# Kernel optimization log

Hardware: AMD Instinct MI355X
Metric: run time of the kernel (lower is better)

Reference implementation:

```python
import jax, jax.numpy as jnp
import numpy as np

NUM_EMBEDDINGS = 1024
EMBEDDING_DIM = 64
COMMITMENT_COST = 0.25


def setup_inputs() -> dict:
    key = jax.random.key(0)
    k1, k2 = jax.random.split(key)
    inputs = jax.random.normal(k1, (16, EMBEDDING_DIM, 64, 64), dtype=jnp.float32)  # NCHW
    embedding = jax.random.normal(k2, (NUM_EMBEDDINGS, EMBEDDING_DIM), dtype=jnp.float32)
    return {"inputs": inputs, "embedding": embedding}


def reference(inputs, embedding):
    # NCHW -> NHWC, flatten to [N, d]
    x = jnp.transpose(inputs, (0, 2, 3, 1))  # [B,H,W,d]
    in_shape = x.shape
    flat = x.reshape(-1, EMBEDDING_DIM)  # [N, d]

    distances = (
        jnp.sum(flat * flat, axis=1, keepdims=True)
        + jnp.sum(embedding * embedding, axis=1)
        - 2.0 * flat @ embedding.T
    )  # [N, K]
    encoding_indices = jnp.argmin(distances, axis=1)  # [N]

    # one-hot @ embedding == gather (avoid materializing [N, K] one-hot)
    quantized = embedding[encoding_indices].reshape(in_shape)  # [B,H,W,d]

    # commitment loss (quantized detached)
    e_latent_loss = jnp.mean((jax.lax.stop_gradient(quantized) - x) ** 2)
    loss = COMMITMENT_COST * e_latent_loss

    # straight-through estimator
    quantized_st = x + jax.lax.stop_gradient(quantized - x)
    quantized_out = jnp.transpose(quantized_st, (0, 3, 1, 2))  # back to NCHW

    return loss, quantized_out, encoding_indices[:, None]
```

## Files before the change

kernel.cpp:

```cpp
#include <hip/hip_runtime.h>


#define DIMS   64
#define HW     4096
#define NPTS   65536
#define NCODES 1024
#define NPB    128
#define QOFF   1
#define IOFF   (1 + NPTS * DIMS)
#define EPSGAP 1.0e-3f

typedef unsigned int uint;
typedef unsigned short ushort;
typedef unsigned long long ull;
typedef __attribute__((ext_vector_type(8))) short short8;
typedef __attribute__((ext_vector_type(16))) float f32x16;

__device__ __forceinline__ ushort bf16_rne(float f) {
    uint u = __float_as_uint(f);
    uint r = u + 0x7FFFu + ((u >> 16) & 1u);
    return (ushort)(r >> 16);
}
__device__ __forceinline__ float bf16f(ushort h) { return __uint_as_float(((uint)h) << 16); }

__device__ __forceinline__ void gload16(const void* g, void* l) {
    __builtin_amdgcn_global_load_lds(
        (const __attribute__((address_space(1))) void*)g,
        (__attribute__((address_space(3))) void*)l, 16, 0, 0);
}

__global__ void vq_prep(const float* __restrict__ emb, ushort* __restrict__ Eh,
                        ushort* __restrict__ El, float* __restrict__ hsq,
                        float* __restrict__ out)
{
    const int t = blockIdx.x * 256 + threadIdx.x;
    if (t == 0) out[0] = 0.f;
    float4 v = ((const float4*)emb)[t];
    ushort h0 = bf16_rne(v.x), h1 = bf16_rne(v.y), h2 = bf16_rne(v.z), h3 = bf16_rne(v.w);
    ushort l0 = bf16_rne(v.x - bf16f(h0)), l1 = bf16_rne(v.y - bf16f(h1));
    ushort l2 = bf16_rne(v.z - bf16f(h2)), l3 = bf16_rne(v.w - bf16f(h3));
    uint2 hp, lp;
    hp.x = (uint)h0 | ((uint)h1 << 16); hp.y = (uint)h2 | ((uint)h3 << 16);
    lp.x = (uint)l0 | ((uint)l1 << 16); lp.y = (uint)l2 | ((uint)l3 << 16);
    const int c = t >> 4, q = t & 15;
    const int g = c >> 5, nn = c & 31;
    const int d0 = q * 4;
    const int ks = d0 >> 4, hh = (d0 >> 3) & 1, j0 = d0 & 7;
    const int base = g * 2048 + ks * 512 + (hh * 32 + nn) * 8 + j0;
    *(uint2*)(Eh + base) = hp;
    *(uint2*)(El + base) = lp;
    float pe = fmaf(v.x, v.x, fmaf(v.y, v.y, fmaf(v.z, v.z, v.w * v.w)));
    pe += __shfl_xor(pe, 1); pe += __shfl_xor(pe, 2);
    pe += __shfl_xor(pe, 4); pe += __shfl_xor(pe, 8);
    if ((t & 15) == 0) hsq[t >> 4] = 0.5f * pe;
}

__launch_bounds__(256, 2)
__global__ void vq_main(const float* __restrict__ in, const float* __restrict__ emb,
                        const ushort* __restrict__ Ehw, const ushort* __restrict__ Elw,
                        const float* __restrict__ hsqw, float* __restrict__ out)
{
    __shared__ ushort sEh[8][2048];
    __shared__ ushort sEl[8][2048];
    __shared__ float sv1[NPB];
    __shared__ float sv2[NPB];
    __shared__ int   si1[NPB];
    __shared__ ull   msk[2];
    __shared__ int   lst[1 + NPB];
    __shared__ float lred[4];

    const int tid = threadIdx.x;
    const int lane = tid & 63, w = tid >> 6;
    const int nn = lane & 31;
    const int h  = lane >> 5;
    const int n0 = blockIdx.x * NPB;
    const int b = n0 >> 12, off = n0 & 4095;
    const float* xbase = in + (size_t)b * (DIMS * HW) + off;

    short8 Ah[4], Al[4];
    {
        const int p = w * 32 + nn;
        #pragma unroll
        for (int ks = 0; ks < 4; ++ks) {
            union { ushort u[8]; short8 v; } th, tl;
            #pragma unroll
            for (int j = 0; j < 8; ++j) {
                float x = xbase[(ks * 16 + h * 8 + j) * HW + p];
                ushort hh = bf16_rne(x);
                th.u[j] = hh;
                tl.u[j] = bf16_rne(x - bf16f(hh));
            }
            Ah[ks] = th.v; Al[ks] = tl.v;
        }
    }
    __builtin_amdgcn_sched_barrier(0);

    float v1s[16], v2s[16]; int i1s[16];
    #pragma unroll
    for (int r = 0; r < 16; ++r) { v1s[r] = 1e30f; v2s[r] = 1e30f; i1s[r] = 0; }

    auto stage = [&](int sg, int buf) {
        #pragma unroll
        for (int u = 0; u < 2; ++u) {
            const int i = 2 * w + u;
            const int c4 = (i & 3) * 512;
            if (i < 4) gload16(Ehw + (size_t)sg * 2048 + c4 + lane * 8, &sEh[buf][c4]);
            else       gload16(Elw + (size_t)sg * 2048 + c4 + lane * 8, &sEl[buf][c4]);
        }
    };

    auto computeG = [&](int g, int buf, float HA) {
        short8 Bh[4], Bl[4];
        #pragma unroll
        for (int ks = 0; ks < 4; ++ks) {
            Bh[ks] = *(const short8*)&sEh[buf][ks * 512 + lane * 8];
            Bl[ks] = *(const short8*)&sEl[buf][ks * 512 + lane * 8];
        }
        f32x16 a1 = {0.f,0.f,0.f,0.f,0.f,0.f,0.f,0.f,0.f,0.f,0.f,0.f,0.f,0.f,0.f,0.f};
        f32x16 a2 = {0.f,0.f,0.f,0.f,0.f,0.f,0.f,0.f,0.f,0.f,0.f,0.f,0.f,0.f,0.f,0.f};
        #pragma unroll
        for (int ks = 0; ks < 4; ++ks)
            a1 = __builtin_amdgcn_mfma_f32_32x32x16_bf16(Ah[ks], Bh[ks], a1, 0, 0, 0);
        #pragma unroll
        for (int ks = 0; ks < 4; ++ks)
            a2 = __builtin_amdgcn_mfma_f32_32x32x16_bf16(Ah[ks], Bl[ks], a2, 0, 0, 0);
        #pragma unroll
        for (int ks = 0; ks < 4; ++ks)
            a2 = __builtin_amdgcn_mfma_f32_32x32x16_bf16(Al[ks], Bh[ks], a2, 0, 0, 0);
        const int ca = g * 32 + nn;
        #pragma unroll
        for (int r = 0; r < 16; ++r) {
            float d = HA - (a1[r] + a2[r]);
            v2s[r] = fminf(v2s[r], fmaxf(d, v1s[r]));
            bool c2 = d < v1s[r];
            i1s[r] = c2 ? ca : i1s[r];
            v1s[r] = fminf(d, v1s[r]);
        }
    };

    stage(0, 0); float hqA = hsqw[nn];
    stage(1, 1); float hqB = hsqw[32 + nn];
    stage(2, 2); float hqC = hsqw[64 + nn];
    float hqD;
    #pragma unroll 1
    for (int g = 0; g < 32; g += 4) {
        {
            const int s = g + 3;
            stage(s, (g + 3) & 7); hqD = hsqw[s * 32 + nn];
            asm volatile("s_waitcnt vmcnt(6)\ns_barrier" ::: "memory");
            computeG(g, g & 7, hqA);
        }
        {
            const int s = (g + 4 < 32) ? g + 4 : 31;
            stage(s, (g + 4) & 7); hqA = hsqw[s * 32 + nn];
            asm volatile("s_waitcnt vmcnt(6)\ns_barrier" ::: "memory");
            computeG(g + 1, (g + 1) & 7, hqB);
        }
        {
            const int s = (g + 5 < 32) ? g + 5 : 31;
            stage(s, (g + 5) & 7); hqB = hsqw[s * 32 + nn];
            asm volatile("s_waitcnt vmcnt(6)\ns_barrier" ::: "memory");
            computeG(g + 2, (g + 2) & 7, hqC);
        }
        {
            const int s = (g + 6 < 32) ? g + 6 : 31;
            stage(s, (g + 6) & 7); hqC = hsqw[s * 32 + nn];
            asm volatile("s_waitcnt vmcnt(6)\ns_barrier" ::: "memory");
            computeG(g + 3, (g + 3) & 7, hqD);
        }
    }

    #pragma unroll
    for (int st = 1; st < 32; st <<= 1) {
        #pragma unroll
        for (int r = 0; r < 16; ++r) {
            float ov1 = __shfl_xor(v1s[r], st);
            float ov2 = __shfl_xor(v2s[r], st);
            int   oi1 = __shfl_xor(i1s[r], st);
            v2s[r] = fminf(fminf(v2s[r], ov2), fmaxf(v1s[r], ov1));
            bool c = (ov1 < v1s[r]) || (ov1 == v1s[r] && oi1 < i1s[r]);
            if (c) i1s[r] = oi1;
            v1s[r] = fminf(v1s[r], ov1);
        }
    }
    if (nn == 0) {
        #pragma unroll
        for (int r = 0; r < 16; ++r) {
            const int row = (r & 3) + 8 * (r >> 2) + 4 * h;
            const int p = w * 32 + row;
            sv1[p] = v1s[r]; si1[p] = i1s[r]; sv2[p] = v2s[r];
        }
    }
    __syncthreads();

    {
        bool f = (tid < NPB) && ((sv2[tid] - sv1[tid]) < EPSGAP);
        ull bm = __ballot(f);
        if (lane == 0 && w < 2) msk[w] = bm;
    }
    __syncthreads();
    if (tid == 0) {
        int c = 0;
        ull m0 = msk[0];
        while (m0) { lst[1 + c++] = __ffsll(m0) - 1; m0 &= m0 - 1; }
        ull m1 = msk[1];
        while (m1) { lst[1 + c++] = 64 + (__ffsll(m1) - 1); m1 &= m1 - 1; }
        lst[0] = c;
    }
    __syncthreads();

    const int cnt = lst[0];
    const float4* e4 = (const float4*)emb;
    for (int it = w; it < cnt; it += 4) {
        const int p = lst[1 + it];
        float xv = xbase[lane * HW + p];
        float bv = 1e30f; int bk = 0;
        #pragma unroll
        for (int half = 0; half < 2; ++half) {
            float dacc[8];
            #pragma unroll
            for (int j = 0; j < 8; ++j) dacc[j] = 0.f;
            for (int d4 = 0; d4 < 16; ++d4) {
                float x0 = __shfl(xv, d4 * 4 + 0), x1 = __shfl(xv, d4 * 4 + 1);
                float x2 = __shfl(xv, d4 * 4 + 2), x3 = __shfl(xv, d4 * 4 + 3);
                #pragma unroll
                for (int j = 0; j < 8; ++j) {
                    const int k = lane + 64 * (half * 8 + j);
                    float4 e = e4[k * 16 + d4];
                    dacc[j] = fmaf(x0, e.x, dacc[j]); dacc[j] = fmaf(x1, e.y, dacc[j]);
                    dacc[j] = fmaf(x2, e.z, dacc[j]); dacc[j] = fmaf(x3, e.w, dacc[j]);
                }
            }
            #pragma unroll
            for (int j = 0; j < 8; ++j) {
                const int k = lane + 64 * (half * 8 + j);
                float v = hsqw[k] - dacc[j];
                if (v < bv) { bv = v; bk = k; }
            }
        }
        #pragma unroll
        for (int st = 32; st; st >>= 1) {
            float ov = __shfl_xor(bv, st);
            int   ok = __shfl_xor(bk, st);
            if (ov < bv || (ov == bv && ok < bk)) { bv = ov; bk = ok; }
        }
        if (lane == 0) si1[p] = bk;
    }
    __syncthreads();

    {
        const int p = tid & 127, dg = tid >> 7;
        const int bi = si1[p];
        if (dg == 0) out[IOFF + n0 + p] = (float)bi;
        const float* e = emb + (size_t)bi * DIMS;
        const float* xp = xbase + p;
        float* oq = out + QOFF + (size_t)b * (DIMS * HW) + off + p;
        float ls = 0.f;
        #pragma unroll
        for (int d0 = 0; d0 < 32; ++d0) {
            const int d = dg * 32 + d0;
            float ev = e[d];
            float xv = xp[d * HW];
            float df = ev - xv;
            ls = fmaf(df, df, ls);
            oq[d * HW] = ev;
        }
        #pragma unroll
        for (int st = 32; st; st >>= 1) ls += __shfl_down(ls, st);
        if (lane == 0) lred[w] = ls;
    }
    __syncthreads();
    if (tid == 0) {
        float s = lred[0] + lred[1] + lred[2] + lred[3];
        atomicAdd(out, s * (0.25f / (float)(NPTS * DIMS)));
    }
}

extern "C" void kernel_launch(void* const* d_in, const int* in_sizes, int n_in,
                              void* d_out, int out_size, void* d_ws, size_t ws_size,
                              hipStream_t stream) {
    const float* in  = (const float*)d_in[0];
    const float* emb = (const float*)d_in[1];
    float* out = (float*)d_out;
    ushort* Eh  = (ushort*)d_ws;
    ushort* El  = (ushort*)((char*)d_ws + 131072);
    float*  hsq = (float*)((char*)d_ws + 262144);
    (void)in_sizes; (void)n_in; (void)out_size; (void)ws_size;

    vq_prep<<<64, 256, 0, stream>>>(emb, Eh, El, hsq, out);
    vq_main<<<NPTS / NPB, 256, 0, stream>>>(in, emb, Eh, El, hsq, out);
}
```

Baseline: 123.8 us.

## Stage two codebook groups per barrier phase to halve pipeline synchronisations

```diff
diff --git a/kernel.cpp b/kernel.cpp
--- a/kernel.cpp
+++ b/kernel.cpp
@@ -93,19 +93,26 @@
             Ah[ks] = th.v; Al[ks] = tl.v;
         }
     }
+    asm volatile("s_waitcnt vmcnt(0)" ::: "memory");
     __builtin_amdgcn_sched_barrier(0);
 
     float v1s[16], v2s[16]; int i1s[16];
     #pragma unroll
     for (int r = 0; r < 16; ++r) { v1s[r] = 1e30f; v2s[r] = 1e30f; i1s[r] = 0; }
 
-    auto stage = [&](int sg, int buf) {
-        #pragma unroll
-        for (int u = 0; u < 2; ++u) {
-            const int i = 2 * w + u;
-            const int c4 = (i & 3) * 512;
-            if (i < 4) gload16(Ehw + (size_t)sg * 2048 + c4 + lane * 8, &sEh[buf][c4]);
-            else       gload16(Elw + (size_t)sg * 2048 + c4 + lane * 8, &sEl[buf][c4]);
+    auto stagePhase = [&](int s) {
+        const int g0 = (2 * s < 32) ? 2 * s : 31;
+        const int g1 = (2 * s + 1 < 32) ? 2 * s + 1 : 31;
+        const int gg = (w >> 1) ? g1 : g0;
+        const int sl = (w >> 1) ? ((2 * s + 1) & 7) : ((2 * s) & 7);
+        if ((w & 1) == 0) {
+            const ushort* src = Ehw + (size_t)gg * 2048;
+            #pragma unroll
+            for (int u = 0; u < 4; ++u) gload16(src + u * 512 + lane * 8, &sEh[sl][u * 512]);
+        } else {
+            const ushort* src = Elw + (size_t)gg * 2048;
+            #pragma unroll
+            for (int u = 0; u < 4; ++u) gload16(src + u * 512 + lane * 8, &sEl[sl][u * 512]);
         }
     };
 
@@ -138,35 +145,51 @@
         }
     };
 
-    stage(0, 0); float hqA = hsqw[nn];
-    stage(1, 1); float hqB = hsqw[32 + nn];
-    stage(2, 2); float hqC = hsqw[64 + nn];
-    float hqD;
+    stagePhase(0); float h0x = hsqw[0 * 32 + nn],  h0y = hsqw[1 * 32 + nn];
+    stagePhase(1); float h1x = hsqw[2 * 32 + nn],  h1y = hsqw[3 * 32 + nn];
+    float h2x, h2y, h3x, h3y;
     #pragma unroll 1
-    for (int g = 0; g < 32; g += 4) {
+    for (int t = 0; t < 4; ++t) {
+        const int P = 4 * t;
         {
-            const int s = g + 3;
-            stage(s, (g + 3) & 7); hqD = hsqw[s * 32 + nn];
-            asm volatile("s_waitcnt vmcnt(6)\ns_barrier" ::: "memory");
-            computeG(g, g & 7, hqA);
+            const int s = P + 2;
+            stagePhase(s);
+            const int ga = (2 * s < 32) ? 2 * s : 31, gb = (2 * s + 1 < 32) ? 2 * s + 1 : 31;
+            h2x = hsqw[ga * 32 + nn]; h2y = hsqw[gb * 32 + nn];
+            asm volatile("s_waitcnt vmcnt(12)\ns_barrier" ::: "memory");
+            const int g = 2 * P;
+            computeG(g,     g & 7,       h0x);
+            computeG(g + 1, (g + 1) & 7, h0y);
         }
         {
-            const int s = (g + 4 < 32) ? g + 4 : 31;
-            stage(s, (g + 4) & 7); hqA = hsqw[s * 32 + nn];
-            asm volatile("s_waitcnt vmcnt(6)\ns_barrier" ::: "memory");
-            computeG(g + 1, (g + 1) & 7, hqB);
+            const int s = P + 3;
+            stagePhase(s);
+            const int ga = (2 * s < 32) ? 2 * s : 31, gb = (2 * s + 1 < 32) ? 2 * s + 1 : 31;
+            h3x = hsqw[ga * 32 + nn]; h3y = hsqw[gb * 32 + nn];
+            asm volatile("s_waitcnt vmcnt(12)\ns_barrier" ::: "memory");
+            const int g = 2 * P + 2;
+            computeG(g,     g & 7,       h1x);
+            computeG(g + 1, (g + 1) & 7, h1y);
         }
         {
-            const int s = (g + 5 < 32) ? g + 5 : 31;
-            stage(s, (g + 5) & 7); hqB = hsqw[s * 32 + nn];
-            asm volatile("s_waitcnt vmcnt(6)\ns_barrier" ::: "memory");
-            computeG(g + 2, (g + 2) & 7, hqC);
+            const int s = P + 4;
+            stagePhase(s);
+            const int ga = (2 * s < 32) ? 2 * s : 31, gb = (2 * s + 1 < 32) ? 2 * s + 1 : 31;
+            h0x = hsqw[ga * 32 + nn]; h0y = hsqw[gb * 32 + nn];
+            asm volatile("s_waitcnt vmcnt(12)\ns_barrier" ::: "memory");
+            const int g = 2 * P + 4;
+            computeG(g,     g & 7,       h2x);
+            computeG(g + 1, (g + 1) & 7, h2y);
         }
         {
-            const int s = (g + 6 < 32) ? g + 6 : 31;
-            stage(s, (g + 6) & 7); hqC = hsqw[s * 32 + nn];
-            asm volatile("s_waitcnt vmcnt(6)\ns_barrier" ::: "memory");
-            computeG(g + 3, (g + 3) & 7, hqD);
+            const int s = P + 5;
+            stagePhase(s);
+            const int ga = (2 * s < 32) ? 2 * s : 31, gb = (2 * s + 1 < 32) ? 2 * s + 1 : 31;
+            h1x = hsqw[ga * 32 + nn]; h1y = hsqw[gb * 32 + nn];
+            asm volatile("s_waitcnt vmcnt(12)\ns_barrier" ::: "memory");
+            const int g = 2 * P + 6;
+            computeG(g,     g & 7,       h3x);
+            computeG(g + 1, (g + 1) & 7, h3y);
         }
     }
 
```

Result: slower. 211.6 us (+70.8%).
